# Performance work log

Measured on AMD Instinct MI355X. Metric: run time of the kernel, lower is better.

## Reference

```python
import jax, jax.numpy as jnp
import numpy as np

HEADS = 8
TOPK = 32
LN_EPS = 1e-5


def _ln(x, g, b):
    m = jnp.mean(x, axis=-1, keepdims=True)
    v = jnp.var(x, axis=-1, keepdims=True)
    return (x - m) * jax.lax.rsqrt(v + LN_EPS) * g + b


def _split_heads(t):
    B, N, I = t.shape
    return t.reshape(B, N, HEADS, I // HEADS).transpose(0, 2, 1, 3)


def _merge_heads(t):
    B, H, N, D = t.shape
    return t.transpose(0, 2, 1, 3).reshape(B, N, H * D)


def _mha(xq, xkv, wq, wk, wv, wo, bo):
    # standard softmax cross-attention (SDPA branch, topk<=0), scale=1/sqrt(d_head)
    q = _split_heads(xq @ wq)
    k = _split_heads(xkv @ wk)
    v = _split_heads(xkv @ wv)
    scale = q.shape[-1] ** -0.5
    attn = jax.nn.softmax(jnp.einsum('bhnd,bhmd->bhnm', q, k) * scale, axis=-1)
    o = jnp.einsum('bhnm,bhmd->bhnd', attn, v)
    return _merge_heads(o) @ wo + bo


def _topk_attn(x, wq, wk, wv, wo, bo):
    # top-k sparse self-attention branch: softmax over the k largest logits per query,
    # all other attention weights are exactly zero -> equivalent to gathering the
    # selected value rows and contracting (avoids materializing the scattered matrix).
    q = _split_heads(x @ wq)
    k = _split_heads(x @ wk)
    v = _split_heads(x @ wv)
    scale = q.shape[-1] ** -0.5
    dots = jnp.einsum('bhnd,bhmd->bhnm', q, k) * scale  # [B,H,N,N]
    top_dots, top_inds = jax.lax.top_k(dots, TOPK)      # [B,H,N,K]
    top_attn = jax.nn.softmax(top_dots, axis=-1)
    # v_sel[b,h,n,k,d] = v[b,h,top_inds[b,h,n,k],d]
    v_sel = jnp.take_along_axis(v[:, :, None, :, :], top_inds[..., None], axis=3)
    o = jnp.einsum('bhnk,bhnkd->bhnd', top_attn, v_sel)
    return _merge_heads(o) @ wo + bo


def _geglu_ff(x, w1, b1, w2, b2):
    h = x @ w1 + b1
    a, g = jnp.split(h, 2, axis=-1)
    return (a * jax.nn.gelu(g, approximate=False)) @ w2 + b2


def _forward(x, context,
             ctx_wq, ctx_wk, ctx_wv, ctx_wo, ctx_bo, cn_g, cn_b,
             im_wq, im_wk, im_wv, im_wo, im_bo,
             xc_wq, xc_wk, xc_wv, xc_wo, xc_bo,
             ffc_w1, ffc_b1, ffc_w2, ffc_b2,
             ffi_w1, ffi_b1, ffi_w2, ffi_b2,
             n1_g, n1_b, n2_g, n2_b, n3_g, n3_b):
    # context self-attention (nx_enhanced=1) + context feed-forward
    cn = _ln(context, cn_g, cn_b)
    c = context + _mha(cn, cn, ctx_wq, ctx_wk, ctx_wv, ctx_wo, ctx_bo)
    c = c + _geglu_ff(c, ffc_w1, ffc_b1, ffc_w2, ffc_b2)
    # image-token top-k sparse self-attention
    h = x + _topk_attn(_ln(x, n1_g, n1_b), im_wq, im_wk, im_wv, im_wo, im_bo)
    # image -> context cross-attention
    h = h + _mha(_ln(h, n2_g, n2_b), c, xc_wq, xc_wk, xc_wv, xc_wo, xc_bo)
    # image feed-forward (GEGLU)
    h = h + _geglu_ff(_ln(h, n3_g, n3_b), ffi_w1, ffi_b1, ffi_w2, ffi_b2)
    return h


def setup_inputs() -> dict:
    key = jax.random.key(0)
    ki = iter(jax.random.split(key, 64))
    def w(*shape):
        return jax.random.normal(next(ki), shape, jnp.float32) * 0.02
    C, D, I = 768, 512, 512
    inp = dict(
        x=jax.random.normal(next(ki), (2, 2304, D), jnp.float32),
        context=jax.random.normal(next(ki), (2, 256, C), jnp.float32),
        spatial_shapes=jnp.array([[48, 48]], dtype=jnp.int32),  # 48*48 == 2304
        ctx_wq=w(C, I), ctx_wk=w(C, I), ctx_wv=w(C, I), ctx_wo=w(I, C),
        ctx_bo=jnp.zeros((C,), jnp.float32),
        cn_g=jnp.ones((C,), jnp.float32), cn_b=jnp.zeros((C,), jnp.float32),
        im_wq=w(D, I), im_wk=w(D, I), im_wv=w(D, I), im_wo=w(I, D),
        im_bo=jnp.zeros((D,), jnp.float32),
        xc_wq=w(D, I), xc_wk=w(C, I), xc_wv=w(C, I), xc_wo=w(I, D),
        xc_bo=jnp.zeros((D,), jnp.float32),
        ffc_w1=w(C, 8 * C), ffc_b1=jnp.zeros((8 * C,), jnp.float32),
        ffc_w2=w(4 * C, C), ffc_b2=jnp.zeros((C,), jnp.float32),
        ffi_w1=w(D, 8 * D), ffi_b1=jnp.zeros((8 * D,), jnp.float32),
        ffi_w2=w(4 * D, D), ffi_b2=jnp.zeros((D,), jnp.float32),
        n1_g=jnp.ones((D,), jnp.float32), n1_b=jnp.zeros((D,), jnp.float32),
        n2_g=jnp.ones((D,), jnp.float32), n2_b=jnp.zeros((D,), jnp.float32),
        n3_g=jnp.ones((D,), jnp.float32), n3_b=jnp.zeros((D,), jnp.float32),
    )
    return inp


def reference(x, context, spatial_shapes,
              ctx_wq, ctx_wk, ctx_wv, ctx_wo, ctx_bo, cn_g, cn_b,
              im_wq, im_wk, im_wv, im_wo, im_bo,
              xc_wq, xc_wk, xc_wv, xc_wo, xc_bo,
              ffc_w1, ffc_b1, ffc_w2, ffc_b2,
              ffi_w1, ffi_b1, ffi_w2, ffi_b2,
              n1_g, n1_b, n2_g, n2_b, n3_g, n3_b):
    del spatial_shapes  # only consumed by the (disabled) deformable path
    return _forward(x, context,
                    ctx_wq, ctx_wk, ctx_wv, ctx_wo, ctx_bo, cn_g, cn_b,
                    im_wq, im_wk, im_wv, im_wo, im_bo,
                    xc_wq, xc_wk, xc_wv, xc_wo, xc_bo,
                    ffc_w1, ffc_b1, ffc_w2, ffc_b2,
                    ffi_w1, ffi_b1, ffi_w2, ffi_b2,
                    n1_g, n1_b, n2_g, n2_b, n3_g, n3_b)
```

## Files before the change

### kernel.cpp

```cpp
#include <hip/hip_runtime.h>
#include <hip/hip_bf16.h>
#include <hip/hip_fp16.h>
#include <cmath>

typedef unsigned short u16;
typedef unsigned long long ull;
typedef __attribute__((ext_vector_type(8))) short short8;
typedef __attribute__((ext_vector_type(4))) float f32x4;
typedef __attribute__((ext_vector_type(4))) unsigned short u16x4;

__device__ __forceinline__ u16 f2bf(float x) {
    unsigned u = __float_as_uint(x);
    u += 0x7fffu + ((u >> 16) & 1u);
    return (u16)(u >> 16);
}
__device__ __forceinline__ float bf2f(u16 b) {
    return __uint_as_float(((unsigned)b) << 16);
}

__device__ __forceinline__ unsigned h2key(unsigned hb) {
    return (hb & 0x8000u) ? (hb ^ 0xFFFFu) : (hb | 0x8000u);
}
__device__ __forceinline__ float key2f(unsigned k) {
    unsigned hb = (k & 0x8000u) ? (k ^ 0x8000u) : (k ^ 0xFFFFu);
    return __half2float(__ushort_as_half((unsigned short)hb));
}

typedef __attribute__((address_space(3))) unsigned int as3_uint;
typedef __attribute__((address_space(1))) unsigned int as1_uint;
__device__ __forceinline__ void gload_lds16(const u16* g, u16* l) {
    __builtin_amdgcn_global_load_lds(
        (as1_uint*)(unsigned long long)(const void*)g,
        (as3_uint*)(unsigned int)(unsigned long long)(const void*)l,
        16, 0, 0);
}

__device__ __forceinline__ float gelu_exact(float g) {
    return 0.5f * g * (1.f + erff(g * 0.70710678118654752f));
}

struct TBatch {
    const float* src[16];
    u16* dst[16];
    int K[16];
    int N[16];
    int start[17];
};

__global__ void k_transpose_cast_batch(TBatch tb) {
    __shared__ float tile[32][33];
    int t = blockIdx.x;
    int m = 0;
    while (t >= tb.start[m + 1]) ++m;
    int rel = t - tb.start[m];
    const int K = tb.K[m], N = tb.N[m];
    const int ntx = N >> 5;
    const int n0 = (rel % ntx) * 32, k0 = (rel / ntx) * 32;
    const float* __restrict__ in = tb.src[m];
    u16* __restrict__ out = tb.dst[m];
    int tx = threadIdx.x, ty = threadIdx.y;
#pragma unroll
    for (int j = 0; j < 4; ++j)
        tile[ty + j * 8][tx] = in[(size_t)(k0 + ty + j * 8) * N + n0 + tx];
    __syncthreads();
#pragma unroll
    for (int j = 0; j < 4; ++j)
        out[(size_t)(n0 + ty + j * 8) * K + k0 + tx] = f2bf(tile[tx][ty + j * 8]);
}

__global__ void k_vtrans16(const u16* __restrict__ in, int stride, int coloff,
                           u16* __restrict__ out) {
    __shared__ int tile[32][33];
    int tx = threadIdx.x, ty = threadIdx.y;
    int d0 = blockIdx.x * 32, k0 = blockIdx.y * 32, b = blockIdx.z;
#pragma unroll
    for (int j = 0; j < 4; ++j)
        tile[ty + j * 8][tx] = in[(size_t)(b * 256 + k0 + ty + j * 8) * stride + coloff + d0 + tx];
    __syncthreads();
#pragma unroll
    for (int j = 0; j < 4; ++j)
        out[(size_t)(b * 512 + d0 + ty + j * 8) * 256 + k0 + tx] = (u16)tile[tx][ty + j * 8];
}

__global__ __launch_bounds__(256)
void k_ln_bf16(const float* __restrict__ in, const float* __restrict__ gam,
               const float* __restrict__ bet, u16* __restrict__ out, int F) {
    int lane = threadIdx.x & 63, w = threadIdx.x >> 6;
    int row = blockIdx.x * 4 + w;
    const int F4 = F >> 2;
    const float4* r4 = reinterpret_cast<const float4*>(in + (size_t)row * F);
    const float4* g4 = reinterpret_cast<const float4*>(gam);
    const float4* b4 = reinterpret_cast<const float4*>(bet);
    float s = 0.f, s2 = 0.f;
    for (int j = lane; j < F4; j += 64) {
        float4 v = r4[j];
        s += v.x + v.y + v.z + v.w;
        s2 += v.x * v.x + v.y * v.y + v.z * v.z + v.w * v.w;
    }
#pragma unroll
    for (int off = 32; off; off >>= 1) { s += __shfl_xor(s, off); s2 += __shfl_xor(s2, off); }
    float mean = s / F;
    float var  = s2 / F - mean * mean;
    float inv  = 1.f / sqrtf(var + 1e-5f);
    u16x4* o4 = reinterpret_cast<u16x4*>(out + (size_t)row * F);
    for (int j = lane; j < F4; j += 64) {
        float4 v = r4[j], gm = g4[j], bt = b4[j];
        u16x4 o;
        o[0] = f2bf((v.x - mean) * inv * gm.x + bt.x);
        o[1] = f2bf((v.y - mean) * inv * gm.y + bt.y);
        o[2] = f2bf((v.z - mean) * inv * gm.z + bt.z);
        o[3] = f2bf((v.w - mean) * inv * gm.w + bt.w);
        o4[j] = o;
    }
}

template <int BM, int BN>
__global__ __launch_bounds__(256)
void gemm_bt(const u16* __restrict__ A, const u16* __restrict__ Bt,
             const float* __restrict__ bias, const float* __restrict__ res,
             float* __restrict__ out32, u16* __restrict__ out16,
             int M, int N, int K) {
    constexpr int WM = BM / 2, WN = BN / 2, FM = WM / 16, FN = WN / 16;
    __shared__ __align__(16) u16 As[BM * 32];
    __shared__ __align__(16) u16 Bs[BN * 32];
    const int tid = threadIdx.x;
    const int lane = tid & 63;
    const int wid = tid >> 6;
    const int wr = wid >> 1, wc = wid & 1;
    const int nwg = gridDim.x * gridDim.y;
    int lin = blockIdx.y * gridDim.x + blockIdx.x;
    lin = (lin & 7) * (nwg >> 3) + (lin >> 3);
    const int m0 = (lin / gridDim.x) * BM, n0 = (lin % gridDim.x) * BN;
    const int r16 = lane & 15;
    const int g8  = (lane >> 4) * 8;
    const int w16 = wid * 16;
    const int ln4 = lane >> 2;
    const int cb8 = (lane & 3) * 8;

    const f32x4 zero4 = {0.f, 0.f, 0.f, 0.f};
    f32x4 acc[FM][FN];
#pragma unroll
    for (int m = 0; m < FM; ++m)
#pragma unroll
        for (int n = 0; n < FN; ++n) acc[m][n] = zero4;

    for (int k0 = 0; k0 < K; k0 += 32) {
#pragma unroll
        for (int p = 0; p < BM / 64; ++p) {
            const int rb = p * 64 + w16;
            gload_lds16(A + (size_t)(m0 + rb + ln4) * K + k0 + cb8, &As[rb * 32]);
        }
#pragma unroll
        for (int p = 0; p < BN / 64; ++p) {
            const int rb = p * 64 + w16;
            gload_lds16(Bt + (size_t)(n0 + rb + ln4) * K + k0 + cb8, &Bs[rb * 32]);
        }
        __syncthreads();
        short8 af[FM], bfr[FN];
#pragma unroll
        for (int m = 0; m < FM; ++m)
            af[m] = *reinterpret_cast<const short8*>(&As[(wr * WM + m * 16 + r16) * 32 + g8]);
#pragma unroll
        for (int n = 0; n < FN; ++n)
            bfr[n] = *reinterpret_cast<const short8*>(&Bs[(wc * WN + n * 16 + r16) * 32 + g8]);
#pragma unroll
        for (int m = 0; m < FM; ++m)
#pragma unroll
            for (int n = 0; n < FN; ++n)
                acc[m][n] = __builtin_amdgcn_mfma_f32_16x16x32_bf16(af[m], bfr[n], acc[m][n], 0, 0, 0);
        __syncthreads();
    }

    const int rg = (lane >> 4) * 4;
#pragma unroll
    for (int m = 0; m < FM; ++m) {
#pragma unroll
        for (int n = 0; n < FN; ++n) {
#pragma unroll
            for (int j = 0; j < 4; ++j) {
                int row = m0 + wr * WM + m * 16 + rg + j;
                int col = n0 + wc * WN + n * 16 + r16;
                float v = acc[m][n][j];
                if (bias) v += bias[col];
                size_t off = (size_t)row * N + col;
                if (res) v += res[off];
                if (out32) out32[off] = v;
                if (out16) out16[off] = f2bf(v);
            }
        }
    }
}

template <int BM>
__global__ __launch_bounds__(256)
void gemm_geglu(const u16* __restrict__ A, const u16* __restrict__ Bt,
                const float* __restrict__ bias, u16* __restrict__ out16,
                int M, int Nh, int K) {
    constexpr int WM = BM / 2, FM = WM / 16;
    __shared__ __align__(16) u16 As[BM * 32];
    __shared__ __align__(16) u16 Bs[128 * 32];
    const int tid = threadIdx.x;
    const int lane = tid & 63;
    const int wid = tid >> 6;
    const int wr = wid >> 1, wc = wid & 1;
    const int nwg = gridDim.x * gridDim.y;
    int lin = blockIdx.y * gridDim.x + blockIdx.x;
    lin = (lin & 7) * (nwg >> 3) + (lin >> 3);
    const int m0 = (lin / gridDim.x) * BM, n0 = (lin % gridDim.x) * 64;
    const int r16 = lane & 15;
    const int g8  = (lane >> 4) * 8;
    const int w16 = wid * 16;
    const int ln4 = lane >> 2;
    const int cb8 = (lane & 3) * 8;

    const f32x4 zero4 = {0.f, 0.f, 0.f, 0.f};
    f32x4 acc_a[FM][2], acc_g[FM][2];
#pragma unroll
    for (int m = 0; m < FM; ++m)
#pragma unroll
        for (int n = 0; n < 2; ++n) { acc_a[m][n] = zero4; acc_g[m][n] = zero4; }

    for (int k0 = 0; k0 < K; k0 += 32) {
#pragma unroll
        for (int p = 0; p < BM / 64; ++p) {
            const int rb = p * 64 + w16;
            gload_lds16(A + (size_t)(m0 + rb + ln4) * K + k0 + cb8, &As[rb * 32]);
        }
        gload_lds16(Bt + (size_t)(n0 + w16 + ln4) * K + k0 + cb8, &Bs[w16 * 32]);
        gload_lds16(Bt + (size_t)(Nh + n0 + w16 + ln4) * K + k0 + cb8, &Bs[(64 + w16) * 32]);
        __syncthreads();
        short8 af[FM], ba[2], bg[2];
#pragma unroll
        for (int m = 0; m < FM; ++m)
            af[m] = *reinterpret_cast<const short8*>(&As[(wr * WM + m * 16 + r16) * 32 + g8]);
#pragma unroll
        for (int n = 0; n < 2; ++n) {
            ba[n] = *reinterpret_cast<const short8*>(&Bs[(wc * 32 + n * 16 + r16) * 32 + g8]);
            bg[n] = *reinterpret_cast<const short8*>(&Bs[(64 + wc * 32 + n * 16 + r16) * 32 + g8]);
        }
#pragma unroll
        for (int m = 0; m < FM; ++m)
#pragma unroll
            for (int n = 0; n < 2; ++n) {
                acc_a[m][n] = __builtin_amdgcn_mfma_f32_16x16x32_bf16(af[m], ba[n], acc_a[m][n], 0, 0, 0);
                acc_g[m][n] = __builtin_amdgcn_mfma_f32_16x16x32_bf16(af[m], bg[n], acc_g[m][n], 0, 0, 0);
            }
        __syncthreads();
    }

    const int rg = (lane >> 4) * 4;
#pragma unroll
    for (int m = 0; m < FM; ++m) {
#pragma unroll
        for (int n = 0; n < 2; ++n) {
#pragma unroll
            for (int j = 0; j < 4; ++j) {
                int row = m0 + wr * WM + m * 16 + rg + j;
                int col = n0 + wc * 32 + n * 16 + r16;
                float a = acc_a[m][n][j] + bias[col];
                float g = acc_g[m][n][j] + bias[Nh + col];
                out16[(size_t)row * Nh + col] = f2bf(a * gelu_exact(g));
            }
        }
    }
}

__global__ __launch_bounds__(256)
void k_attn_mfma(const u16* __restrict__ Qb, int sq, const u16* __restrict__ Kb,
                 int sk, const u16* __restrict__ VT, u16* __restrict__ out, int NQ) {
    __shared__ float sc[16][268];
    __shared__ u16   pb[16][268];
    const int tid = threadIdx.x, lane = tid & 63, w = tid >> 6;
    const int nqb = NQ >> 4;
    const int h = blockIdx.x & 7;
    const int rest = blockIdx.x >> 3;
    const int b = rest / nqb;
    const int q0 = (rest % nqb) << 4;
    const int r16 = lane & 15, g8 = (lane >> 4) * 8, rq = (lane >> 4) * 4;

    const size_t qrow = ((size_t)(b * NQ + q0 + r16)) * sq + h * 64;
    const short8 af0 = *reinterpret_cast<const short8*>(Qb + qrow + g8);
    const short8 af1 = *reinterpret_cast<const short8*>(Qb + qrow + 32 + g8);
    const u16* kb = Kb + (size_t)b * 256 * sk + h * 64;
    const f32x4 zero4 = {0.f, 0.f, 0.f, 0.f};
#pragma unroll
    for (int t = 0; t < 4; ++t) {
        const size_t krow = (size_t)(t * 64 + w * 16 + r16) * sk;
        const short8 bf0 = *reinterpret_cast<const short8*>(kb + krow + g8);
        const short8 bf1 = *reinterpret_cast<const short8*>(kb + krow + 32 + g8);
        f32x4 acc = __builtin_amdgcn_mfma_f32_16x16x32_bf16(af0, bf0, zero4, 0, 0, 0);
        acc = __builtin_amdgcn_mfma_f32_16x16x32_bf16(af1, bf1, acc, 0, 0, 0);
        const int col = t * 64 + w * 16 + r16;
#pragma unroll
        for (int j = 0; j < 4; ++j) sc[rq + j][col] = acc[j] * 0.125f;
    }
    __syncthreads();
#pragma unroll
    for (int qi = 0; qi < 4; ++qi) {
        const int q = w * 4 + qi;
        float4 v = *reinterpret_cast<const float4*>(&sc[q][lane * 4]);
        float m = fmaxf(fmaxf(v.x, v.y), fmaxf(v.z, v.w));
#pragma unroll
        for (int off = 32; off; off >>= 1) m = fmaxf(m, __shfl_xor(m, off));
        float e0 = expf(v.x - m), e1 = expf(v.y - m), e2 = expf(v.z - m), e3 = expf(v.w - m);
        float sum = e0 + e1 + e2 + e3;
#pragma unroll
        for (int off = 32; off; off >>= 1) sum += __shfl_xor(sum, off);
        float inv = 1.f / sum;
        u16x4 p4;
        p4[0] = f2bf(e0 * inv); p4[1] = f2bf(e1 * inv);
        p4[2] = f2bf(e2 * inv); p4[3] = f2bf(e3 * inv);
        *reinterpret_cast<u16x4*>(&pb[q][lane * 4]) = p4;
    }
    __syncthreads();
    f32x4 o = zero4;
    const u16* vt = VT + ((size_t)(b * 512 + h * 64 + w * 16 + r16)) * 256;
#pragma unroll
    for (int kk = 0; kk < 8; ++kk) {
        const short8 pa = *reinterpret_cast<const short8*>(&pb[r16][kk * 32 + g8]);
        const short8 vv = *reinterpret_cast<const short8*>(vt + kk * 32 + g8);
        o = __builtin_amdgcn_mfma_f32_16x16x32_bf16(pa, vv, o, 0, 0, 0);
    }
#pragma unroll
    for (int j = 0; j < 4; ++j)
        out[((size_t)(b * NQ + q0 + rq + j)) * 512 + h * 64 + w * 16 + r16] = f2bf(o[j]);
}

__global__ __launch_bounds__(256)
void gemm_scores(const u16* __restrict__ QKV, u16* __restrict__ keys) {
    __shared__ __align__(16) u16 As[2][128 * 32];
    __shared__ __align__(16) u16 Bs[2][128 * 32];
    const int tid = threadIdx.x;
    const int lane = tid & 63;
    const int wid = tid >> 6;
    const int wr = wid >> 1, wc = wid & 1;
    int lin = blockIdx.x;
    lin = (lin & 7) * 648 + (lin >> 3);
    const int bh = lin / 324;
    const int rel = lin % 324;
    const int m0 = (rel / 18) * 128, n0 = (rel % 18) * 128;
    const int b = bh >> 3, h = bh & 7;
    const u16* Qb = QKV + (size_t)b * 2304 * 1536 + h * 64;
    const u16* Kb = Qb + 512;
    const int r16 = lane & 15;
    const int g8  = (lane >> 4) * 8;
    const int w16 = wid * 16;
    const int ln4 = lane >> 2;
    const int cb8 = (lane & 3) * 8;

#pragma unroll
    for (int kk = 0; kk < 2; ++kk) {
#pragma unroll
        for (int p = 0; p < 2; ++p) {
            const int rb = p * 64 + w16;
            gload_lds16(Qb + (size_t)(m0 + rb + ln4) * 1536 + kk * 32 + cb8, &As[kk][rb * 32]);
            gload_lds16(Kb + (size_t)(n0 + rb + ln4) * 1536 + kk * 32 + cb8, &Bs[kk][rb * 32]);
        }
    }
    __syncthreads();

    const f32x4 zero4 = {0.f, 0.f, 0.f, 0.f};
    f32x4 acc[4][4];
#pragma unroll
    for (int m = 0; m < 4; ++m)
#pragma unroll
        for (int n = 0; n < 4; ++n) acc[m][n] = zero4;

    short8 af[2][4], bfr[2][4];
#pragma unroll
    for (int kk = 0; kk < 2; ++kk)
#pragma unroll
        for (int m = 0; m < 4; ++m) {
            af[kk][m] = *reinterpret_cast<const short8*>(&As[kk][(wr * 64 + m * 16 + r16) * 32 + g8]);
            bfr[kk][m] = *reinterpret_cast<const short8*>(&Bs[kk][(wc * 64 + m * 16 + r16) * 32 + g8]);
        }
#pragma unroll
    for (int kk = 0; kk < 2; ++kk)
#pragma unroll
        for (int m = 0; m < 4; ++m)
#pragma unroll
            for (int n = 0; n < 4; ++n)
                acc[m][n] = __builtin_amdgcn_mfma_f32_16x16x32_bf16(af[kk][m], bfr[kk][n], acc[m][n], 0, 0, 0);

    u16* kout = keys + (size_t)bh * 2304 * 2304;
    const int rg = (lane >> 4) * 4;
#pragma unroll
    for (int m = 0; m < 4; ++m) {
#pragma unroll
        for (int n = 0; n < 4; ++n) {
#pragma unroll
            for (int j = 0; j < 4; ++j) {
                int row = m0 + wr * 64 + m * 16 + rg + j;
                int col = n0 + wc * 64 + n * 16 + r16;
                unsigned hb = __half_as_ushort(__float2half(acc[m][n][j] * 0.125f));
                kout[(size_t)row * 2304 + col] = (u16)h2key(hb);
            }
        }
    }
}

__global__ __launch_bounds__(256)
void k_topk_sel(const u16* __restrict__ keys, const u16* __restrict__ QKV,
                u16* __restrict__ out) {
    __shared__ int   ilist[4][32];
    __shared__ float wlist[4][32];
    const int tid = threadIdx.x, lane = tid & 63, w = tid >> 6;
    const int h = blockIdx.x & 7;
    const int t7 = blockIdx.x >> 3;
    const int b = t7 / 576;
    const int q = (t7 % 576) * 4 + w;

    const u16* krow = keys + ((size_t)((b * 8 + h) * 2304) + q) * 2304;
    const ull ltm = (1ull << lane) - 1ull;
    unsigned ka[9], kb[9], kc[9], kd[9];
#pragma unroll
    for (int j = 0; j < 9; ++j) {
        const uint2 v = *reinterpret_cast<const uint2*>(krow + j * 256 + lane * 4);
        ka[j] = v.x & 0xFFFFu; kb[j] = v.x >> 16;
        kc[j] = v.y & 0xFFFFu; kd[j] = v.y >> 16;
    }

    unsigned thr = 0;
    for (int bit = 15; bit >= 0; --bit) {
        const unsigned cand = thr | (1u << bit);
        unsigned c0 = 0, c1 = 0, c2 = 0, c3 = 0;
#pragma unroll
        for (int j = 0; j < 9; ++j) {
            c0 += (ka[j] >= cand) ? 1u : 0u;
            c1 += (kb[j] >= cand) ? 1u : 0u;
            c2 += (kc[j] >= cand) ? 1u : 0u;
            c3 += (kd[j] >= cand) ? 1u : 0u;
        }
        unsigned c = (c0 + c1) + (c2 + c3);
#pragma unroll
        for (int off = 32; off; off >>= 1) c += (unsigned)__shfl_xor((int)c, off);
        if (c >= 32) { thr = cand; if (c == 32) break; }
    }

    int tot = 0;
#pragma unroll
    for (int j = 0; j < 9; ++j) {
        const ull m0 = __ballot(ka[j] > thr);
        const ull m1 = __ballot(kb[j] > thr);
        const ull m2 = __ballot(kc[j] > thr);
        const ull m3 = __ballot(kd[j] > thr);
        const int p0 = (int)__popcll(m0), p1 = (int)__popcll(m1);
        const int p2 = (int)__popcll(m2), p3 = (int)__popcll(m3);
        if (ka[j] > thr) {
            int pos = tot + (int)__popcll(m0 & ltm);
            ilist[w][pos] = j * 256 + lane * 4 + 0; wlist[w][pos] = key2f(ka[j]);
        }
        if (kb[j] > thr) {
            int pos = tot + p0 + (int)__popcll(m1 & ltm);
            ilist[w][pos] = j * 256 + lane * 4 + 1; wlist[w][pos] = key2f(kb[j]);
        }
        if (kc[j] > thr) {
            int pos = tot + p0 + p1 + (int)__popcll(m2 & ltm);
            ilist[w][pos] = j * 256 + lane * 4 + 2; wlist[w][pos] = key2f(kc[j]);
        }
        if (kd[j] > thr) {
            int pos = tot + p0 + p1 + p2 + (int)__popcll(m3 & ltm);
            ilist[w][pos] = j * 256 + lane * 4 + 3; wlist[w][pos] = key2f(kd[j]);
        }
        tot += p0 + p1 + p2 + p3;
    }
    const int r = 32 - tot;
    if (r > 0) {
        const float tv = key2f(thr);
        int t2 = 0;
#pragma unroll
        for (int j = 0; j < 9; ++j) {
            const ull m0 = __ballot(ka[j] == thr);
            const ull m1 = __ballot(kb[j] == thr);
            const ull m2 = __ballot(kc[j] == thr);
            const ull m3 = __ballot(kd[j] == thr);
            const int base = (int)__popcll(m0 & ltm) + (int)__popcll(m1 & ltm) +
                             (int)__popcll(m2 & ltm) + (int)__popcll(m3 & ltm);
            const int b0 = (int)((m0 >> lane) & 1ull);
            const int b1 = b0 + (int)((m1 >> lane) & 1ull);
            const int b2 = b1 + (int)((m2 >> lane) & 1ull);
            if (ka[j] == thr) {
                int pos = t2 + base;
                if (pos < r) { ilist[w][tot + pos] = j * 256 + lane * 4 + 0; wlist[w][tot + pos] = tv; }
            }
            if (kb[j] == thr) {
                int pos = t2 + base + b0;
                if (pos < r) { ilist[w][tot + pos] = j * 256 + lane * 4 + 1; wlist[w][tot + pos] = tv; }
            }
            if (kc[j] == thr) {
                int pos = t2 + base + b1;
                if (pos < r) { ilist[w][tot + pos] = j * 256 + lane * 4 + 2; wlist[w][tot + pos] = tv; }
            }
            if (kd[j] == thr) {
                int pos = t2 + base + b2;
                if (pos < r) { ilist[w][tot + pos] = j * 256 + lane * 4 + 3; wlist[w][tot + pos] = tv; }
            }
            t2 += (int)__popcll(m0) + (int)__popcll(m1) +
                  (int)__popcll(m2) + (int)__popcll(m3);
        }
    }
    float wv = (lane < 32) ? wlist[w][lane] : -3.0e38f;
    float mf = wv;
#pragma unroll
    for (int off = 32; off; off >>= 1) mf = fmaxf(mf, __shfl_xor(mf, off));
    float e = (lane < 32) ? expf(wv - mf) : 0.f;
    float sum = e;
#pragma unroll
    for (int off = 32; off; off >>= 1) sum += __shfl_xor(sum, off);
    if (lane < 32) wlist[w][lane] = e / sum;
    const u16* vb = QKV + (size_t)b * 2304 * 1536 + 1024 + h * 64 + lane;
    u16 vr[32];
#pragma unroll
    for (int i = 0; i < 32; ++i)
        vr[i] = vb[(size_t)ilist[w][i] * 1536];
    float o = 0.f;
#pragma unroll
    for (int i = 0; i < 32; ++i)
        o += wlist[w][i] * bf2f(vr[i]);
    out[((size_t)(b * 2304 + q)) * 512 + h * 64 + lane] = f2bf(o);
}

static constexpr size_t O_WQKVC = 0;
static constexpr size_t O_WOC   = O_WQKVC + 2359296;
static constexpr size_t O_W1C   = O_WOC + 786432;
static constexpr size_t O_W2C   = O_W1C + 9437184;
static constexpr size_t O_WQKVI = O_W2C + 4718592;
static constexpr size_t O_WOI   = O_WQKVI + 1572864;
static constexpr size_t O_WQX   = O_WOI + 524288;
static constexpr size_t O_WKVX  = O_WQX + 524288;
static constexpr size_t O_WOX   = O_WKVX + 1572864;
static constexpr size_t O_W1I   = O_WOX + 524288;
static constexpr size_t O_W2I   = O_W1I + 4194304;
static constexpr size_t O_CF16  = O_W2I + 2097152;
static constexpr size_t O_H     = O_CF16 + 786432;
static constexpr size_t O_H2    = O_H + 9437184;
static constexpr size_t O_S     = O_H2 + 9437184;
static constexpr size_t O_CN16  = O_S;
static constexpr size_t O_QKVC  = O_CN16 + 786432;
static constexpr size_t O_VTC   = O_QKVC + 1572864;
static constexpr size_t O_AO16  = O_VTC + 524288;
static constexpr size_t O_CBUF  = O_AO16 + 524288;
static constexpr size_t O_C16   = O_CBUF + 1572864;
static constexpr size_t O_AG16  = O_C16 + 786432;
static constexpr size_t O_XLN   = O_S;
static constexpr size_t O_QKVI  = O_XLN + 4718592;
static constexpr size_t O_KEYS  = O_QKVI + 14155776;
static constexpr size_t O_TO16  = O_KEYS + 169869312;
static constexpr size_t O_H2LN  = O_S;
static constexpr size_t O_XQ    = O_H2LN + 4718592;
static constexpr size_t O_KVX   = O_XQ + 4718592;
static constexpr size_t O_VTX   = O_KVX + 1048576;
static constexpr size_t O_XO16  = O_VTX + 524288;
static constexpr size_t O_H3    = O_S;
static constexpr size_t O_AGI   = O_H3 + 4718592;

extern "C" void kernel_launch(void* const* d_in, const int* in_sizes, int n_in,
                              void* d_out, int out_size, void* d_ws, size_t ws_size,
                              hipStream_t stream) {
    (void)in_sizes; (void)n_in; (void)out_size; (void)ws_size;
    const float* x      = (const float*)d_in[0];
    const float* ctx    = (const float*)d_in[1];
    const float* ctx_wq = (const float*)d_in[3];
    const float* ctx_wk = (const float*)d_in[4];
    const float* ctx_wv = (const float*)d_in[5];
    const float* ctx_wo = (const float*)d_in[6];
    const float* ctx_bo = (const float*)d_in[7];
    const float* cn_g   = (const float*)d_in[8];
    const float* cn_b   = (const float*)d_in[9];
    const float* im_wq  = (const float*)d_in[10];
    const float* im_wk  = (const float*)d_in[11];
    const float* im_wv  = (const float*)d_in[12];
    const float* im_wo  = (const float*)d_in[13];
    const float* im_bo  = (const float*)d_in[14];
    const float* xc_wq  = (const float*)d_in[15];
    const float* xc_wk  = (const float*)d_in[16];
    const float* xc_wv  = (const float*)d_in[17];
    const float* xc_wo  = (const float*)d_in[18];
    const float* xc_bo  = (const float*)d_in[19];
    const float* ffc_w1 = (const float*)d_in[20];
    const float* ffc_b1 = (const float*)d_in[21];
    const float* ffc_w2 = (const float*)d_in[22];
    const float* ffc_b2 = (const float*)d_in[23];
    const float* ffi_w1 = (const float*)d_in[24];
    const float* ffi_b1 = (const float*)d_in[25];
    const float* ffi_w2 = (const float*)d_in[26];
    const float* ffi_b2 = (const float*)d_in[27];
    const float* n1_g   = (const float*)d_in[28];
    const float* n1_b   = (const float*)d_in[29];
    const float* n2_g   = (const float*)d_in[30];
    const float* n2_b   = (const float*)d_in[31];
    const float* n3_g   = (const float*)d_in[32];
    const float* n3_b   = (const float*)d_in[33];
    char* ws = (char*)d_ws;
    float* out = (float*)d_out;
    auto Wp = [&](size_t off) { return (u16*)(ws + off); };
    auto Fp = [&](size_t off) { return (float*)(ws + off); };
    dim3 tb(32, 8);

    TBatch tbat;
    const float* srcs[16] = {ctx_wq, ctx_wk, ctx_wv, ctx_wo, ffc_w1, ffc_w2,
                             im_wq, im_wk, im_wv, im_wo, xc_wq, xc_wk, xc_wv,
                             xc_wo, ffi_w1, ffi_w2};
    const size_t dsts[16] = {O_WQKVC, O_WQKVC + 786432, O_WQKVC + 1572864, O_WOC,
                             O_W1C, O_W2C,
                             O_WQKVI, O_WQKVI + 524288, O_WQKVI + 1048576, O_WOI,
                             O_WQX, O_WKVX, O_WKVX + 786432, O_WOX,
                             O_W1I, O_W2I};
    const int Ks[16] = {768, 768, 768, 512, 768, 3072, 512, 512, 512, 512,
                        512, 768, 768, 512, 512, 2048};
    const int Ns[16] = {512, 512, 512, 768, 6144, 768, 512, 512, 512, 512,
                        512, 512, 512, 512, 4096, 512};
    int acc = 0;
    for (int i = 0; i < 16; ++i) {
        tbat.src[i] = srcs[i];
        tbat.dst[i] = Wp(dsts[i]);
        tbat.K[i] = Ks[i];
        tbat.N[i] = Ns[i];
        tbat.start[i] = acc;
        acc += (Ns[i] >> 5) * (Ks[i] >> 5);
    }
    tbat.start[16] = acc;
    k_transpose_cast_batch<<<acc, tb, 0, stream>>>(tbat);

    k_ln_bf16<<<128, 256, 0, stream>>>(ctx, cn_g, cn_b, Wp(O_CN16), 768);
    gemm_bt<64, 64><<<dim3(24, 8), 256, 0, stream>>>(Wp(O_CN16), Wp(O_WQKVC), nullptr, nullptr, nullptr, Wp(O_QKVC), 512, 1536, 768);
    k_vtrans16<<<dim3(16, 8, 2), tb, 0, stream>>>(Wp(O_QKVC), 1536, 1024, Wp(O_VTC));
    k_attn_mfma<<<256, 256, 0, stream>>>(Wp(O_QKVC), 1536, Wp(O_QKVC) + 512, 1536, Wp(O_VTC), Wp(O_AO16), 256);
    gemm_bt<64, 64><<<dim3(12, 8), 256, 0, stream>>>(Wp(O_AO16), Wp(O_WOC), ctx_bo, ctx, Fp(O_CBUF), Wp(O_C16), 512, 768, 512);
    gemm_geglu<128><<<dim3(48, 4), 256, 0, stream>>>(Wp(O_C16), Wp(O_W1C), ffc_b1, Wp(O_AG16), 512, 3072, 768);
    gemm_bt<64, 64><<<dim3(12, 8), 256, 0, stream>>>(Wp(O_AG16), Wp(O_W2C), ffc_b2, Fp(O_CBUF), nullptr, Wp(O_CF16), 512, 768, 3072);

    k_ln_bf16<<<1152, 256, 0, stream>>>(x, n1_g, n1_b, Wp(O_XLN), 512);
    gemm_bt<128, 128><<<dim3(12, 36), 256, 0, stream>>>(Wp(O_XLN), Wp(O_WQKVI), nullptr, nullptr, nullptr, Wp(O_QKVI), 4608, 1536, 512);
    gemm_scores<<<5184, 256, 0, stream>>>(Wp(O_QKVI), Wp(O_KEYS));
    k_topk_sel<<<9216, 256, 0, stream>>>(Wp(O_KEYS), Wp(O_QKVI), Wp(O_TO16));
    gemm_bt<128, 64><<<dim3(8, 36), 256, 0, stream>>>(Wp(O_TO16), Wp(O_WOI), im_bo, x, Fp(O_H), nullptr, 4608, 512, 512);

    k_ln_bf16<<<1152, 256, 0, stream>>>(Fp(O_H), n2_g, n2_b, Wp(O_H2LN), 512);
    gemm_bt<128, 64><<<dim3(8, 36), 256, 0, stream>>>(Wp(O_H2LN), Wp(O_WQX), nullptr, nullptr, nullptr, Wp(O_XQ), 4608, 512, 512);
    gemm_bt<64, 64><<<dim3(16, 8), 256, 0, stream>>>(Wp(O_CF16), Wp(O_WKVX), nullptr, nullptr, nullptr, Wp(O_KVX), 512, 1024, 768);
    k_vtrans16<<<dim3(16, 8, 2), tb, 0, stream>>>(Wp(O_KVX), 1024, 512, Wp(O_VTX));
    k_attn_mfma<<<2304, 256, 0, stream>>>(Wp(O_XQ), 512, Wp(O_KVX), 1024, Wp(O_VTX), Wp(O_XO16), 2304);
    gemm_bt<128, 64><<<dim3(8, 36), 256, 0, stream>>>(Wp(O_XO16), Wp(O_WOX), xc_bo, Fp(O_H), Fp(O_H2), nullptr, 4608, 512, 512);

    k_ln_bf16<<<1152, 256, 0, stream>>>(Fp(O_H2), n3_g, n3_b, Wp(O_H3), 512);
    gemm_geglu<128><<<dim3(32, 36), 256, 0, stream>>>(Wp(O_H3), Wp(O_W1I), ffi_b1, Wp(O_AGI), 4608, 2048, 512);
    gemm_bt<128, 64><<<dim3(8, 36), 256, 0, stream>>>(Wp(O_AGI), Wp(O_W2I), ffi_b2, Fp(O_H2), out, nullptr, 4608, 512, 2048);
}
```

Baseline: 494.1 us.

## Pack top-k radix counting into 16-bit SIMD ops and shrink GEMM tiles

The top-k threshold search now keeps the keys packed two per 32-bit register and counts candidates with packed u16 subtract-clamp and min instructions, roughly halving the ALU work per bisection step. The tie-fill pass now skips chunks once enough tied elements have been collected. Separately, four 4608x512 GEMMs switch from 128x64 to 64x64 tiles, doubling the block count for better CU occupancy at the cost of less data reuse per block. The packed counter accumulates two 16-bit lanes, each of which stays below 64k, so it cannot overflow.

```diff
diff --git a/kernel.cpp b/kernel.cpp
--- a/kernel.cpp
+++ b/kernel.cpp
@@ -412,26 +412,27 @@
 
     const u16* krow = keys + ((size_t)((b * 8 + h) * 2304) + q) * 2304;
     const ull ltm = (1ull << lane) - 1ull;
-    unsigned ka[9], kb[9], kc[9], kd[9];
+    unsigned kp[18];
 #pragma unroll
     for (int j = 0; j < 9; ++j) {
         const uint2 v = *reinterpret_cast<const uint2*>(krow + j * 256 + lane * 4);
-        ka[j] = v.x & 0xFFFFu; kb[j] = v.x >> 16;
-        kc[j] = v.y & 0xFFFFu; kd[j] = v.y >> 16;
-    }
-
+        kp[2 * j] = v.x; kp[2 * j + 1] = v.y;
+    }
+
+    const unsigned ones = 0x00010001u;
     unsigned thr = 0;
     for (int bit = 15; bit >= 0; --bit) {
         const unsigned cand = thr | (1u << bit);
-        unsigned c0 = 0, c1 = 0, c2 = 0, c3 = 0;
-#pragma unroll
-        for (int j = 0; j < 9; ++j) {
-            c0 += (ka[j] >= cand) ? 1u : 0u;
-            c1 += (kb[j] >= cand) ? 1u : 0u;
-            c2 += (kc[j] >= cand) ? 1u : 0u;
-            c3 += (kd[j] >= cand) ? 1u : 0u;
-        }
-        unsigned c = (c0 + c1) + (c2 + c3);
+        const unsigned cm1 = (cand - 1) * 0x10001u;
+        unsigned cacc = 0;
+#pragma unroll
+        for (int j = 0; j < 18; ++j) {
+            unsigned s, m;
+            asm("v_pk_sub_u16 %0, %1, %2 clamp" : "=v"(s) : "v"(kp[j]), "v"(cm1));
+            asm("v_pk_min_u16 %0, %1, %2" : "=v"(m) : "v"(s), "v"(ones));
+            cacc += m;
+        }
+        unsigned c = (cacc & 0xFFFFu) + (cacc >> 16);
 #pragma unroll
         for (int off = 32; off; off >>= 1) c += (unsigned)__shfl_xor((int)c, off);
         if (c >= 32) { thr = cand; if (c == 32) break; }
@@ -440,27 +441,30 @@
     int tot = 0;
 #pragma unroll
     for (int j = 0; j < 9; ++j) {
-        const ull m0 = __ballot(ka[j] > thr);
-        const ull m1 = __ballot(kb[j] > thr);
-        const ull m2 = __ballot(kc[j] > thr);
-        const ull m3 = __ballot(kd[j] > thr);
+        const unsigned x = kp[2 * j], y = kp[2 * j + 1];
+        const unsigned ka = x & 0xFFFFu, kb = x >> 16;
+        const unsigned kc = y & 0xFFFFu, kd = y >> 16;
+        const ull m0 = __ballot(ka > thr);
+        const ull m1 = __ballot(kb > thr);
+        const ull m2 = __ballot(kc > thr);
+        const ull m3 = __ballot(kd > thr);
         const int p0 = (int)__popcll(m0), p1 = (int)__popcll(m1);
         const int p2 = (int)__popcll(m2), p3 = (int)__popcll(m3);
-        if (ka[j] > thr) {
+        if (ka > thr) {
             int pos = tot + (int)__popcll(m0 & ltm);
-            ilist[w][pos] = j * 256 + lane * 4 + 0; wlist[w][pos] = key2f(ka[j]);
-        }
-        if (kb[j] > thr) {
+            ilist[w][pos] = j * 256 + lane * 4 + 0; wlist[w][pos] = key2f(ka);
+        }
+        if (kb > thr) {
             int pos = tot + p0 + (int)__popcll(m1 & ltm);
-            ilist[w][pos] = j * 256 + lane * 4 + 1; wlist[w][pos] = key2f(kb[j]);
-        }
-        if (kc[j] > thr) {
+            ilist[w][pos] = j * 256 + lane * 4 + 1; wlist[w][pos] = key2f(kb);
+        }
+        if (kc > thr) {
             int pos = tot + p0 + p1 + (int)__popcll(m2 & ltm);
-            ilist[w][pos] = j * 256 + lane * 4 + 2; wlist[w][pos] = key2f(kc[j]);
-        }
-        if (kd[j] > thr) {
+            ilist[w][pos] = j * 256 + lane * 4 + 2; wlist[w][pos] = key2f(kc);
+        }
+        if (kd > thr) {
             int pos = tot + p0 + p1 + p2 + (int)__popcll(m3 & ltm);
-            ilist[w][pos] = j * 256 + lane * 4 + 3; wlist[w][pos] = key2f(kd[j]);
+            ilist[w][pos] = j * 256 + lane * 4 + 3; wlist[w][pos] = key2f(kd);
         }
         tot += p0 + p1 + p2 + p3;
     }
@@ -470,33 +474,38 @@
         int t2 = 0;
 #pragma unroll
         for (int j = 0; j < 9; ++j) {
-            const ull m0 = __ballot(ka[j] == thr);
-            const ull m1 = __ballot(kb[j] == thr);
-            const ull m2 = __ballot(kc[j] == thr);
-            const ull m3 = __ballot(kd[j] == thr);
-            const int base = (int)__popcll(m0 & ltm) + (int)__popcll(m1 & ltm) +
-                             (int)__popcll(m2 & ltm) + (int)__popcll(m3 & ltm);
-            const int b0 = (int)((m0 >> lane) & 1ull);
-            const int b1 = b0 + (int)((m1 >> lane) & 1ull);
-            const int b2 = b1 + (int)((m2 >> lane) & 1ull);
-            if (ka[j] == thr) {
-                int pos = t2 + base;
-                if (pos < r) { ilist[w][tot + pos] = j * 256 + lane * 4 + 0; wlist[w][tot + pos] = tv; }
+            if (t2 < r) {
+                const unsigned x = kp[2 * j], y = kp[2 * j + 1];
+                const unsigned ka = x & 0xFFFFu, kb = x >> 16;
+                const unsigned kc = y & 0xFFFFu, kd = y >> 16;
+                const ull m0 = __ballot(ka == thr);
+                const ull m1 = __ballot(kb == thr);
+                const ull m2 = __ballot(kc == thr);
+                const ull m3 = __ballot(kd == thr);
+                const int base = (int)__popcll(m0 & ltm) + (int)__popcll(m1 & ltm) +
+                                 (int)__popcll(m2 & ltm) + (int)__popcll(m3 & ltm);
+                const int b0 = (int)((m0 >> lane) & 1ull);
+                const int b1 = b0 + (int)((m1 >> lane) & 1ull);
+                const int b2 = b1 + (int)((m2 >> lane) & 1ull);
+                if (ka == thr) {
+                    int pos = t2 + base;
+                    if (pos < r) { ilist[w][tot + pos] = j * 256 + lane * 4 + 0; wlist[w][tot + pos] = tv; }
+                }
+                if (kb == thr) {
+                    int pos = t2 + base + b0;
+                    if (pos < r) { ilist[w][tot + pos] = j * 256 + lane * 4 + 1; wlist[w][tot + pos] = tv; }
+                }
+                if (kc == thr) {
+                    int pos = t2 + base + b1;
+                    if (pos < r) { ilist[w][tot + pos] = j * 256 + lane * 4 + 2; wlist[w][tot + pos] = tv; }
+                }
+                if (kd == thr) {
+                    int pos = t2 + base + b2;
+                    if (pos < r) { ilist[w][tot + pos] = j * 256 + lane * 4 + 3; wlist[w][tot + pos] = tv; }
+                }
+                t2 += (int)__popcll(m0) + (int)__popcll(m1) +
+                      (int)__popcll(m2) + (int)__popcll(m3);
             }
-            if (kb[j] == thr) {
-                int pos = t2 + base + b0;
-                if (pos < r) { ilist[w][tot + pos] = j * 256 + lane * 4 + 1; wlist[w][tot + pos] = tv; }
-            }
-            if (kc[j] == thr) {
-                int pos = t2 + base + b1;
-                if (pos < r) { ilist[w][tot + pos] = j * 256 + lane * 4 + 2; wlist[w][tot + pos] = tv; }
-            }
-            if (kd[j] == thr) {
-                int pos = t2 + base + b2;
-                if (pos < r) { ilist[w][tot + pos] = j * 256 + lane * 4 + 3; wlist[w][tot + pos] = tv; }
-            }
-            t2 += (int)__popcll(m0) + (int)__popcll(m1) +
-                  (int)__popcll(m2) + (int)__popcll(m3);
         }
     }
     float wv = (lane < 32) ? wlist[w][lane] : -3.0e38f;
@@ -634,16 +643,16 @@
     gemm_bt<128, 128><<<dim3(12, 36), 256, 0, stream>>>(Wp(O_XLN), Wp(O_WQKVI), nullptr, nullptr, nullptr, Wp(O_QKVI), 4608, 1536, 512);
     gemm_scores<<<5184, 256, 0, stream>>>(Wp(O_QKVI), Wp(O_KEYS));
     k_topk_sel<<<9216, 256, 0, stream>>>(Wp(O_KEYS), Wp(O_QKVI), Wp(O_TO16));
-    gemm_bt<128, 64><<<dim3(8, 36), 256, 0, stream>>>(Wp(O_TO16), Wp(O_WOI), im_bo, x, Fp(O_H), nullptr, 4608, 512, 512);
+    gemm_bt<64, 64><<<dim3(8, 72), 256, 0, stream>>>(Wp(O_TO16), Wp(O_WOI), im_bo, x, Fp(O_H), nullptr, 4608, 512, 512);
 
     k_ln_bf16<<<1152, 256, 0, stream>>>(Fp(O_H), n2_g, n2_b, Wp(O_H2LN), 512);
-    gemm_bt<128, 64><<<dim3(8, 36), 256, 0, stream>>>(Wp(O_H2LN), Wp(O_WQX), nullptr, nullptr, nullptr, Wp(O_XQ), 4608, 512, 512);
+    gemm_bt<64, 64><<<dim3(8, 72), 256, 0, stream>>>(Wp(O_H2LN), Wp(O_WQX), nullptr, nullptr, nullptr, Wp(O_XQ), 4608, 512, 512);
     gemm_bt<64, 64><<<dim3(16, 8), 256, 0, stream>>>(Wp(O_CF16), Wp(O_WKVX), nullptr, nullptr, nullptr, Wp(O_KVX), 512, 1024, 768);
     k_vtrans16<<<dim3(16, 8, 2), tb, 0, stream>>>(Wp(O_KVX), 1024, 512, Wp(O_VTX));
     k_attn_mfma<<<2304, 256, 0, stream>>>(Wp(O_XQ), 512, Wp(O_KVX), 1024, Wp(O_VTX), Wp(O_XO16), 2304);
-    gemm_bt<128, 64><<<dim3(8, 36), 256, 0, stream>>>(Wp(O_XO16), Wp(O_WOX), xc_bo, Fp(O_H), Fp(O_H2), nullptr, 4608, 512, 512);
+    gemm_bt<64, 64><<<dim3(8, 72), 256, 0, stream>>>(Wp(O_XO16), Wp(O_WOX), xc_bo, Fp(O_H), Fp(O_H2), nullptr, 4608, 512, 512);
 
     k_ln_bf16<<<1152, 256, 0, stream>>>(Fp(O_H2), n3_g, n3_b, Wp(O_H3), 512);
     gemm_geglu<128><<<dim3(32, 36), 256, 0, stream>>>(Wp(O_H3), Wp(O_W1I), ffi_b1, Wp(O_AGI), 4608, 2048, 512);
-    gemm_bt<128, 64><<<dim3(8, 36), 256, 0, stream>>>(Wp(O_AGI), Wp(O_W2I), ffi_b2, Fp(O_H2), out, nullptr, 4608, 512, 2048);
-}
+    gemm_bt<64, 64><<<dim3(8, 72), 256, 0, stream>>>(Wp(O_AGI), Wp(O_W2I), ffi_b2, Fp(O_H2), out, nullptr, 4608, 512, 2048);
+}
```

Result: faster. 454.5 us (-8.0%).
